# Optimization experiments

Measured on AMD Instinct MI355X. Metric: run time of the kernel, lower is better.

The kernel has to match this reference:

```python
import jax, jax.numpy as jnp
import numpy as np

N_NODES = 50000


def setup_inputs() -> dict:
    key = jax.random.key(0)
    k1, k2 = jax.random.split(key)
    edge_index = jax.random.randint(k1, (2, 800000), 0, N_NODES, dtype=jnp.int64)
    x = jax.random.normal(k2, (N_NODES, 64), dtype=jnp.float32)
    return {"edge_index": edge_index, "x": x}


def reference(edge_index, x):
    # message: x_j = gather x at source nodes edge_index[1]  -> [E, D]
    # aggregate 'add': scatter-add per-edge messages into target nodes edge_index[0]
    # update: identity
    msgs = x[edge_index[1]]  # [E, D]
    out = jax.ops.segment_sum(msgs, edge_index[0], num_segments=x.shape[0])  # [N, D]
    return out
```

## Files before the change

kernel.cpp:

```cpp
#include <hip/hip_runtime.h>
#include <hip/hip_bf16.h>


#define D 64
#define NB2 512
#define GPB_MAX 128
#define CAP 2048
#define EPB 4096
#define PTHR 1024
#define BTHR 1024
#define SPILL_MAX 65536

__global__ void init_kernel(int* __restrict__ brun, int* __restrict__ scnt) {
    int t = threadIdx.x;
    if (t < NB2) brun[t] = t * CAP;
    if (t == NB2) scnt[0] = 0;
}

__global__ __launch_bounds__(PTHR) void part_kernel(const int* __restrict__ tgt,
                                                    const int* __restrict__ src,
                                                    int* __restrict__ brun,
                                                    unsigned* __restrict__ pairs,
                                                    int* __restrict__ spill,
                                                    int* __restrict__ scnt,
                                                    int E, int gpb) {
    __shared__ int h[NB2];
    __shared__ int coff[NB2];
    __shared__ int crun[NB2];
    __shared__ int gbase[NB2];
    __shared__ int a[NB2];
    __shared__ unsigned sw[EPB];
    __shared__ unsigned short sb[EPB];
    int t = threadIdx.x;
    int base = blockIdx.x * EPB;
    for (int i = t; i < NB2; i += PTHR) h[i] = 0;
    __syncthreads();

    int myb[EPB / PTHR];
    unsigned myw[EPB / PTHR];
    #pragma unroll
    for (int k = 0; k < EPB / PTHR; ++k) {
        int e = base + t + k * PTHR;
        int bk = -1; unsigned w = 0;
        if (e < E) {
            unsigned tg = (unsigned)tgt[e];
            unsigned s  = (unsigned)src[e];
            bk = (int)(tg / (unsigned)gpb);
            unsigned lt = tg - (unsigned)bk * (unsigned)gpb;
            w = (lt << 16) | s;
            atomicAdd(&h[bk], 1);
        }
        myb[k] = bk; myw[k] = w;
    }
    __syncthreads();

    if (t < NB2) a[t] = h[t];
    __syncthreads();
    for (int d = 1; d < NB2; d <<= 1) {
        int v = 0;
        if (t < NB2 && t >= d) v = a[t - d];
        __syncthreads();
        if (t < NB2) a[t] += v;
        __syncthreads();
    }
    if (t < NB2) {
        int ex = t ? a[t - 1] : 0;
        coff[t] = ex; crun[t] = ex;
    }
    __syncthreads();

    #pragma unroll
    for (int k = 0; k < EPB / PTHR; ++k) {
        if (myb[k] >= 0) {
            int pos = atomicAdd(&crun[myb[k]], 1);
            sw[pos] = myw[k];
            sb[pos] = (unsigned short)myb[k];
        }
    }
    if (t < NB2) gbase[t] = h[t] ? atomicAdd(&brun[t], h[t]) : 0;
    __syncthreads();

    int nitems = a[NB2 - 1];
    for (int i = t; i < nitems; i += PTHR) {
        int bk = sb[i];
        int dst = gbase[bk] + (i - coff[bk]);
        if (dst < (bk + 1) * CAP) {
            pairs[dst] = sw[i];
        } else {
            int sp = atomicAdd(scnt, 1);
            if (sp < SPILL_MAX) {
                unsigned w = sw[i];
                spill[2 * sp]     = bk * gpb + (int)(w >> 16);
                spill[2 * sp + 1] = (int)(w & 0xffffu);
            }
        }
    }
}

__global__ __launch_bounds__(BTHR) void bsum_kernel(const int* __restrict__ brun,
                                                    const unsigned* __restrict__ pairs,
                                                    const float* __restrict__ x,
                                                    float* __restrict__ out,
                                                    int N, int gpb) {
    __shared__ unsigned sp[CAP];
    __shared__ unsigned short ss[CAP];
    __shared__ int cnt2[GPB_MAX];
    __shared__ int roff[GPB_MAX + 1];
    __shared__ int wpos[GPB_MAX];
    int b = blockIdx.x;
    int t = threadIdx.x;
    int lo = b * gpb;
    if (lo >= N) return;
    int hi = lo + gpb; if (hi > N) hi = N;
    int nn = hi - lo;
    int wid = t >> 6;
    int lane = t & 63;

    int m = brun[b] - b * CAP;
    if (m > CAP) m = CAP;

    for (int i = t; i < m; i += BTHR) sp[i] = pairs[b * CAP + i];
    if (t < GPB_MAX) cnt2[t] = 0;
    __syncthreads();
    for (int i = t; i < m; i += BTHR) atomicAdd(&cnt2[sp[i] >> 16], 1);
    __syncthreads();
    if (wid == 0) {
        int c0 = cnt2[lane], c1 = cnt2[64 + lane];
        int s0c = c0, s1c = c1;
        for (int d2 = 1; d2 < 64; d2 <<= 1) {
            int v = __shfl_up(s0c, d2); if (lane >= d2) s0c += v;
        }
        int tot0 = __shfl(s0c, 63);
        for (int d2 = 1; d2 < 64; d2 <<= 1) {
            int v = __shfl_up(s1c, d2); if (lane >= d2) s1c += v;
        }
        roff[lane] = s0c - c0;        wpos[lane] = s0c - c0;
        roff[64 + lane] = tot0 + s1c - c1;
        wpos[64 + lane] = tot0 + s1c - c1;
        if (lane == 63) roff[GPB_MAX] = tot0 + s1c;
    }
    __syncthreads();
    for (int i = t; i < m; i += BTHR) {
        unsigned w = sp[i];
        int pos = atomicAdd(&wpos[w >> 16], 1);
        ss[pos] = (unsigned short)(w & 0xffffu);
    }
    __syncthreads();

    float acc[8];
    #pragma unroll
    for (int r = 0; r < 8; ++r) acc[r] = 0.f;
    #pragma unroll
    for (int r = 0; r < 8; ++r) {
        int node = wid + (r << 4);
        if (node < nn) {
            int rs = roff[node], re = roff[node + 1];
            float a = acc[r];
            for (int j = rs; j < re; j += 8) {
                int idv[8]; float vv[8];
                #pragma unroll
                for (int k = 0; k < 8; ++k) {
                    int jj = j + k;
                    idv[k] = ss[(jj < re) ? jj : rs];
                }
                #pragma unroll
                for (int k = 0; k < 8; ++k)
                    vv[k] = x[idv[k] * D + lane];
                #pragma unroll
                for (int k = 0; k < 8; ++k)
                    if (j + k < re) a += vv[k];
            }
            acc[r] = a;
        }
    }
    #pragma unroll
    for (int r = 0; r < 8; ++r) {
        int node = wid + (r << 4);
        if (node < nn) out[(size_t)(lo + node) * D + lane] = acc[r];
    }
}

__global__ void spill_kernel(const int* __restrict__ spill,
                             const int* __restrict__ scnt,
                             const float* __restrict__ x,
                             float* __restrict__ out) {
    int n = scnt[0]; if (n > SPILL_MAX) n = SPILL_MAX;
    int lane = threadIdx.x & 63;
    int wave = (int)((blockIdx.x * blockDim.x + threadIdx.x) >> 6);
    int nw = (int)((gridDim.x * blockDim.x) >> 6);
    for (int i = wave; i < n; i += nw) {
        int tg = spill[2 * i], s = spill[2 * i + 1];
        atomicAdd(&out[(size_t)tg * D + lane], x[(size_t)s * D + lane]);
    }
}

__global__ void mp_scatter_add_kernel(const int* __restrict__ tgt,
                                      const int* __restrict__ src,
                                      const float* __restrict__ x,
                                      float* __restrict__ out,
                                      int E) {
    long long tid = (long long)blockIdx.x * blockDim.x + threadIdx.x;
    int e = (int)(tid >> 6);
    int d = (int)(tid & 63);
    if (e >= E) return;
    atomicAdd(&out[(long long)tgt[e] * D + d], x[(long long)src[e] * D + d]);
}

extern "C" void kernel_launch(void* const* d_in, const int* in_sizes, int n_in,
                              void* d_out, int out_size, void* d_ws, size_t ws_size,
                              hipStream_t stream) {
    const int* edge_index = (const int*)d_in[0];
    const float* x        = (const float*)d_in[1];
    float* out            = (float*)d_out;

    int E = in_sizes[0] / 2;
    int N = out_size / D;
    const int* tgt = edge_index;
    const int* src = edge_index + E;

    int gpb = (N + NB2 - 1) / NB2;

    size_t need = (size_t)(NB2 + 4 + NB2 * CAP + 2 * SPILL_MAX) * sizeof(int);

    if (N > 65536 || gpb > GPB_MAX || ws_size < need) {
        hipMemsetAsync(d_out, 0, (size_t)out_size * sizeof(float), stream);
        long long total = (long long)E * D;
        long long grid = (total + 255) / 256;
        mp_scatter_add_kernel<<<(dim3)(unsigned)grid, 256, 0, stream>>>(tgt, src, x, out, E);
        return;
    }

    int* brun = (int*)d_ws;
    int* scnt = brun + NB2;
    unsigned* pairs = (unsigned*)(scnt + 4);
    int* spill = (int*)(pairs + (size_t)NB2 * CAP);

    init_kernel<<<1, NB2 + 64, 0, stream>>>(brun, scnt);
    int GE = (E + EPB - 1) / EPB;
    part_kernel<<<GE, PTHR, 0, stream>>>(tgt, src, brun, pairs, spill, scnt, E, gpb);
    bsum_kernel<<<NB2, BTHR, 0, stream>>>(brun, pairs, x, out, N, gpb);
    spill_kernel<<<64, 256, 0, stream>>>(spill, scnt, x, out);
}
```

Baseline: 47.53 us.

## Fold spill pass into bucket-sum kernel and replace block scan with wave scan

Drops the init kernel in favour of a memset and changes brun to hold bucket-local counts. The 512-bucket prefix sum in the partition kernel becomes a single-wavefront shuffle scan, which removes many block-wide barriers. The separate spill kernel is merged into bsum: after its own work, each block scans the spill list and applies only the entries that fall in its own bucket. This saves two kernel launches, but every block now rereads the whole spill list whenever spills exist.

Result: faster. 46.18 us (-2.8%).

```diff
diff --git a/kernel.cpp b/kernel.cpp
--- a/kernel.cpp
+++ b/kernel.cpp
@@ -10,12 +10,6 @@
 #define PTHR 1024
 #define BTHR 1024
 #define SPILL_MAX 65536
-
-__global__ void init_kernel(int* __restrict__ brun, int* __restrict__ scnt) {
-    int t = threadIdx.x;
-    if (t < NB2) brun[t] = t * CAP;
-    if (t == NB2) scnt[0] = 0;
-}
 
 __global__ __launch_bounds__(PTHR) void part_kernel(const int* __restrict__ tgt,
                                                     const int* __restrict__ src,
@@ -28,11 +22,15 @@
     __shared__ int coff[NB2];
     __shared__ int crun[NB2];
     __shared__ int gbase[NB2];
-    __shared__ int a[NB2];
     __shared__ unsigned sw[EPB];
     __shared__ unsigned short sb[EPB];
     int t = threadIdx.x;
+    int wid = t >> 6, lane = t & 63;
     int base = blockIdx.x * EPB;
+    int nitems = E - base;
+    if (nitems > EPB) nitems = EPB;
+    if (nitems < 0) nitems = 0;
+
     for (int i = t; i < NB2; i += PTHR) h[i] = 0;
     __syncthreads();
 
@@ -40,32 +38,41 @@
     unsigned myw[EPB / PTHR];
     #pragma unroll
     for (int k = 0; k < EPB / PTHR; ++k) {
-        int e = base + t + k * PTHR;
-        int bk = -1; unsigned w = 0;
-        if (e < E) {
+        myb[k] = -1; myw[k] = 0;
+        int j = t + k * PTHR;
+        if (j < nitems) {
+            int e = base + j;
             unsigned tg = (unsigned)tgt[e];
             unsigned s  = (unsigned)src[e];
-            bk = (int)(tg / (unsigned)gpb);
-            unsigned lt = tg - (unsigned)bk * (unsigned)gpb;
-            w = (lt << 16) | s;
+            int bk = (int)(tg / (unsigned)gpb);
+            myb[k] = bk;
+            myw[k] = ((tg - (unsigned)bk * (unsigned)gpb) << 16) | s;
             atomicAdd(&h[bk], 1);
         }
-        myb[k] = bk; myw[k] = w;
-    }
-    __syncthreads();
-
-    if (t < NB2) a[t] = h[t];
-    __syncthreads();
-    for (int d = 1; d < NB2; d <<= 1) {
-        int v = 0;
-        if (t < NB2 && t >= d) v = a[t - d];
-        __syncthreads();
-        if (t < NB2) a[t] += v;
-        __syncthreads();
+    }
+    __syncthreads();
+
+    if (wid == 0) {
+        int b8 = lane * 8;
+        int cvals[8], pre[8], s = 0;
+        #pragma unroll
+        for (int k = 0; k < 8; ++k) { cvals[k] = h[b8 + k]; pre[k] = s; s += cvals[k]; }
+        int run = s;
+        #pragma unroll
+        for (int d2 = 1; d2 < 64; d2 <<= 1) {
+            int v = __shfl_up(run, d2); if (lane >= d2) run += v;
+        }
+        int excl = run - s;
+        #pragma unroll
+        for (int k = 0; k < 8; ++k) {
+            int v2 = excl + pre[k];
+            coff[b8 + k] = v2;
+            crun[b8 + k] = v2;
+        }
     }
     if (t < NB2) {
-        int ex = t ? a[t - 1] : 0;
-        coff[t] = ex; crun[t] = ex;
+        int hv = h[t];
+        gbase[t] = hv ? atomicAdd(&brun[t], hv) : 0;
     }
     __syncthreads();
 
@@ -77,21 +84,19 @@
             sb[pos] = (unsigned short)myb[k];
         }
     }
-    if (t < NB2) gbase[t] = h[t] ? atomicAdd(&brun[t], h[t]) : 0;
-    __syncthreads();
-
-    int nitems = a[NB2 - 1];
+    __syncthreads();
+
     for (int i = t; i < nitems; i += PTHR) {
         int bk = sb[i];
-        int dst = gbase[bk] + (i - coff[bk]);
-        if (dst < (bk + 1) * CAP) {
-            pairs[dst] = sw[i];
+        int dstl = gbase[bk] + (i - coff[bk]);
+        if (dstl < CAP) {
+            pairs[bk * CAP + dstl] = sw[i];
         } else {
-            int sp = atomicAdd(scnt, 1);
-            if (sp < SPILL_MAX) {
+            int sp2 = atomicAdd(scnt, 1);
+            if (sp2 < SPILL_MAX) {
                 unsigned w = sw[i];
-                spill[2 * sp]     = bk * gpb + (int)(w >> 16);
-                spill[2 * sp + 1] = (int)(w & 0xffffu);
+                spill[2 * sp2]     = bk * gpb + (int)(w >> 16);
+                spill[2 * sp2 + 1] = (int)(w & 0xffffu);
             }
         }
     }
@@ -99,6 +104,8 @@
 
 __global__ __launch_bounds__(BTHR) void bsum_kernel(const int* __restrict__ brun,
                                                     const unsigned* __restrict__ pairs,
+                                                    const int* __restrict__ spill,
+                                                    const int* __restrict__ scnt,
                                                     const float* __restrict__ x,
                                                     float* __restrict__ out,
                                                     int N, int gpb) {
@@ -109,88 +116,89 @@
     __shared__ int wpos[GPB_MAX];
     int b = blockIdx.x;
     int t = threadIdx.x;
-    int lo = b * gpb;
-    if (lo >= N) return;
-    int hi = lo + gpb; if (hi > N) hi = N;
-    int nn = hi - lo;
     int wid = t >> 6;
     int lane = t & 63;
-
-    int m = brun[b] - b * CAP;
-    if (m > CAP) m = CAP;
-
-    for (int i = t; i < m; i += BTHR) sp[i] = pairs[b * CAP + i];
-    if (t < GPB_MAX) cnt2[t] = 0;
-    __syncthreads();
-    for (int i = t; i < m; i += BTHR) atomicAdd(&cnt2[sp[i] >> 16], 1);
-    __syncthreads();
-    if (wid == 0) {
-        int c0 = cnt2[lane], c1 = cnt2[64 + lane];
-        int s0c = c0, s1c = c1;
-        for (int d2 = 1; d2 < 64; d2 <<= 1) {
-            int v = __shfl_up(s0c, d2); if (lane >= d2) s0c += v;
-        }
-        int tot0 = __shfl(s0c, 63);
-        for (int d2 = 1; d2 < 64; d2 <<= 1) {
-            int v = __shfl_up(s1c, d2); if (lane >= d2) s1c += v;
-        }
-        roff[lane] = s0c - c0;        wpos[lane] = s0c - c0;
-        roff[64 + lane] = tot0 + s1c - c1;
-        wpos[64 + lane] = tot0 + s1c - c1;
-        if (lane == 63) roff[GPB_MAX] = tot0 + s1c;
-    }
-    __syncthreads();
-    for (int i = t; i < m; i += BTHR) {
-        unsigned w = sp[i];
-        int pos = atomicAdd(&wpos[w >> 16], 1);
-        ss[pos] = (unsigned short)(w & 0xffffu);
-    }
-    __syncthreads();
-
-    float acc[8];
-    #pragma unroll
-    for (int r = 0; r < 8; ++r) acc[r] = 0.f;
-    #pragma unroll
-    for (int r = 0; r < 8; ++r) {
-        int node = wid + (r << 4);
-        if (node < nn) {
-            int rs = roff[node], re = roff[node + 1];
-            float a = acc[r];
-            for (int j = rs; j < re; j += 8) {
-                int idv[8]; float vv[8];
-                #pragma unroll
-                for (int k = 0; k < 8; ++k) {
-                    int jj = j + k;
-                    idv[k] = ss[(jj < re) ? jj : rs];
+    int lo = b * gpb;
+
+    if (lo < N) {
+        int hi = lo + gpb; if (hi > N) hi = N;
+        int nn = hi - lo;
+        int m = brun[b];
+        if (m > CAP) m = CAP;
+
+        for (int i = t; i < m; i += BTHR) sp[i] = pairs[b * CAP + i];
+        if (t < GPB_MAX) cnt2[t] = 0;
+        __syncthreads();
+        for (int i = t; i < m; i += BTHR) atomicAdd(&cnt2[sp[i] >> 16], 1);
+        __syncthreads();
+        if (wid == 0) {
+            int c0 = cnt2[lane], c1 = cnt2[64 + lane];
+            int s0c = c0, s1c = c1;
+            #pragma unroll
+            for (int d2 = 1; d2 < 64; d2 <<= 1) {
+                int v = __shfl_up(s0c, d2); if (lane >= d2) s0c += v;
+            }
+            int tot0 = __shfl(s0c, 63);
+            #pragma unroll
+            for (int d2 = 1; d2 < 64; d2 <<= 1) {
+                int v = __shfl_up(s1c, d2); if (lane >= d2) s1c += v;
+            }
+            roff[lane] = s0c - c0;        wpos[lane] = s0c - c0;
+            roff[64 + lane] = tot0 + s1c - c1;
+            wpos[64 + lane] = tot0 + s1c - c1;
+            if (lane == 63) roff[GPB_MAX] = tot0 + s1c;
+        }
+        __syncthreads();
+        for (int i = t; i < m; i += BTHR) {
+            unsigned w = sp[i];
+            int pos = atomicAdd(&wpos[w >> 16], 1);
+            ss[pos] = (unsigned short)(w & 0xffffu);
+        }
+        __syncthreads();
+
+        float acc[8];
+        #pragma unroll
+        for (int r = 0; r < 8; ++r) acc[r] = 0.f;
+        #pragma unroll
+        for (int r = 0; r < 8; ++r) {
+            int node = wid + (r << 4);
+            if (node < nn) {
+                int rs = roff[node], re = roff[node + 1];
+                float a = acc[r];
+                for (int j = rs; j < re; j += 8) {
+                    int idv[8]; float vv[8];
+                    #pragma unroll
+                    for (int k = 0; k < 8; ++k) {
+                        int jj = j + k;
+                        idv[k] = ss[(jj < re) ? jj : rs];
+                    }
+                    #pragma unroll
+                    for (int k = 0; k < 8; ++k)
+                        vv[k] = x[idv[k] * D + lane];
+                    #pragma unroll
+                    for (int k = 0; k < 8; ++k)
+                        if (j + k < re) a += vv[k];
                 }
-                #pragma unroll
-                for (int k = 0; k < 8; ++k)
-                    vv[k] = x[idv[k] * D + lane];
-                #pragma unroll
-                for (int k = 0; k < 8; ++k)
-                    if (j + k < re) a += vv[k];
-            }
-            acc[r] = a;
-        }
-    }
-    #pragma unroll
-    for (int r = 0; r < 8; ++r) {
-        int node = wid + (r << 4);
-        if (node < nn) out[(size_t)(lo + node) * D + lane] = acc[r];
-    }
-}
-
-__global__ void spill_kernel(const int* __restrict__ spill,
-                             const int* __restrict__ scnt,
-                             const float* __restrict__ x,
-                             float* __restrict__ out) {
+                acc[r] = a;
+            }
+        }
+        #pragma unroll
+        for (int r = 0; r < 8; ++r) {
+            int node = wid + (r << 4);
+            if (node < nn) out[(size_t)(lo + node) * D + lane] = acc[r];
+        }
+    }
+
+    __syncthreads();
     int n = scnt[0]; if (n > SPILL_MAX) n = SPILL_MAX;
-    int lane = threadIdx.x & 63;
-    int wave = (int)((blockIdx.x * blockDim.x + threadIdx.x) >> 6);
-    int nw = (int)((gridDim.x * blockDim.x) >> 6);
-    for (int i = wave; i < n; i += nw) {
-        int tg = spill[2 * i], s = spill[2 * i + 1];
-        atomicAdd(&out[(size_t)tg * D + lane], x[(size_t)s * D + lane]);
+    if (n > 0) {
+        for (int i = wid; i < n; i += 16) {
+            int tg2 = spill[2 * i];
+            if (tg2 / gpb == b) {
+                int s2 = spill[2 * i + 1];
+                atomicAdd(&out[(size_t)tg2 * D + lane], x[(size_t)s2 * D + lane]);
+            }
+        }
     }
 }
 
@@ -220,7 +228,7 @@
 
     int gpb = (N + NB2 - 1) / NB2;
 
-    size_t need = (size_t)(NB2 + 4 + NB2 * CAP + 2 * SPILL_MAX) * sizeof(int);
+    size_t need = (size_t)(NB2 + 4 + (size_t)NB2 * CAP + 2 * SPILL_MAX) * sizeof(int);
 
     if (N > 65536 || gpb > GPB_MAX || ws_size < need) {
         hipMemsetAsync(d_out, 0, (size_t)out_size * sizeof(float), stream);
@@ -235,9 +243,9 @@
     unsigned* pairs = (unsigned*)(scnt + 4);
     int* spill = (int*)(pairs + (size_t)NB2 * CAP);
 
-    init_kernel<<<1, NB2 + 64, 0, stream>>>(brun, scnt);
+    hipMemsetAsync(brun, 0, (NB2 + 4) * sizeof(int), stream);
+
     int GE = (E + EPB - 1) / EPB;
     part_kernel<<<GE, PTHR, 0, stream>>>(tgt, src, brun, pairs, spill, scnt, E, gpb);
-    bsum_kernel<<<NB2, BTHR, 0, stream>>>(brun, pairs, x, out, N, gpb);
-    spill_kernel<<<64, 256, 0, stream>>>(spill, scnt, x, out);
-}
+    bsum_kernel<<<NB2, BTHR, 0, stream>>>(brun, pairs, spill, scnt, x, out, N, gpb);
+}
```
